# Performance work log

Measured on AMD Instinct MI355X. Metric: run time of the kernel, lower is better.

Reference implementation:

```python
import jax, jax.numpy as jnp
import numpy as np

B, Nq, Nk, R = 4, 1024, 1024, 256
NH, DK, DV = 8, 64, 64


def setup_inputs() -> dict:
    key = jax.random.key(0)
    ks = jax.random.split(key, 16)
    mk = lambda k, shape, s=1.0: jax.random.normal(k, shape, dtype=jnp.float32) * s
    inp = {
        'Q_real': mk(ks[0], (B, Nq, R)), 'Q_imag': mk(ks[1], (B, Nq, R)),
        'K_real': mk(ks[2], (B, Nk, R)), 'K_imag': mk(ks[3], (B, Nk, R)),
        'V_real': mk(ks[4], (B, Nk, R)), 'V_imag': mk(ks[5], (B, Nk, R)),
        'WQ_r': mk(ks[6], (NH * DK, R), 0.02), 'WQ_i': mk(ks[7], (NH * DK, R), 0.02),
        'WK_r': mk(ks[8], (NH * DK, R), 0.02), 'WK_i': mk(ks[9], (NH * DK, R), 0.02),
        'WV_r': mk(ks[10], (NH * DV, R), 0.02), 'WV_i': mk(ks[11], (NH * DV, R), 0.02),
        'WO_r': mk(ks[12], (R, NH * DV), 0.02), 'WO_i': mk(ks[13], (R, NH * DV), 0.02),
        'mask': jax.random.randint(ks[14], (B, Nk), 0, 2).astype(bool),
    }
    return inp


def _complex_linear(x, w_r, w_i):
    # x: complex [..., in]; weights real [out, in]. Same math as 4 real matmuls.
    w = (w_r + 1j * w_i).astype(jnp.complex64)
    return x @ w.T


def reference(Q_real, Q_imag, K_real, K_imag, V_real, V_imag,
              WQ_r, WQ_i, WK_r, WK_i, WV_r, WV_i, WO_r, WO_i, mask):
    Q = (Q_real + 1j * Q_imag).astype(jnp.complex64)
    K = (K_real + 1j * K_imag).astype(jnp.complex64)
    V = (V_real + 1j * V_imag).astype(jnp.complex64)

    Qp = _complex_linear(Q, WQ_r, WQ_i).reshape(B, Nq, NH, DK).transpose(0, 2, 1, 3)
    Kp = _complex_linear(K, WK_r, WK_i).reshape(B, Nk, NH, DK).transpose(0, 2, 1, 3)
    Vp = _complex_linear(V, WV_r, WV_i).reshape(B, Nk, NH, DV).transpose(0, 2, 1, 3)

    # complex scores [B, NH, Nq, Nk]; conj on K matches torch .conj().transpose
    scores = jnp.einsum('bhqd,bhkd->bhqk', Qp, jnp.conj(Kp)) / jnp.sqrt(jnp.float32(DK))
    scores_abs = jnp.abs(scores)

    m = mask[:, None, None, :]                    # [B,1,1,Nk]
    valid = jnp.any(mask, axis=-1)[:, None, None, None]  # [B,1,1,1] valid query rows
    masked = jnp.where(m, scores_abs, -jnp.inf)
    # avoid all -inf rows feeding softmax (those rows are zeroed afterwards)
    safe = jnp.where(valid, masked, 0.0)
    w = jax.nn.softmax(safe, axis=-1)
    w = jnp.where(valid, w, 0.0)

    attn = jnp.einsum('bhqk,bhkd->bhqd', w.astype(Vp.dtype), Vp)
    attn = attn.transpose(0, 2, 1, 3).reshape(B, Nq, NH * DV)
    return _complex_linear(attn, WO_r, WO_i)
```

## Files before the change

### kernel.cpp

```cpp
#include <hip/hip_runtime.h>
#include <hip/hip_bf16.h>

#define NBATCH 4
#define NSEQ   1024
#define RD     256
#define NHEAD  8
#define HD     64
#define NHD    512

typedef __attribute__((ext_vector_type(8))) short  short8;
typedef __attribute__((ext_vector_type(4))) short  short4v;
typedef __attribute__((ext_vector_type(4))) float  float4v;

#define MFMA16(a,b,c) __builtin_amdgcn_mfma_f32_16x16x32_bf16(a,b,c,0,0,0)

typedef const void __attribute__((address_space(1)))* gas_t;
typedef void __attribute__((address_space(3)))* las_t;
#define GLOAD16(g, l) __builtin_amdgcn_global_load_lds((gas_t)(g), (las_t)(l), 16, 0, 0)

static __device__ __forceinline__ short f2b(float f) {
    __hip_bfloat16 h = __float2bfloat16(f);
    union { __hip_bfloat16 h; short s; } u; u.h = h;
    return u.s;
}
static __device__ __forceinline__ void st4(short* dst, float4v v) {
    short4v p;
    p[0] = f2b(v[0]); p[1] = f2b(v[1]);
    p[2] = f2b(v[2]); p[3] = f2b(v[3]);
    *(short4v*)dst = p;
}

struct ConvArgs { const float* src[15]; short* dst[15]; int n4[15]; };

__global__ __launch_bounds__(256) void convert_bf16(ConvArgs ca)
{
    const int a = blockIdx.y;
    if (a == 14) {
        if (blockIdx.x != 0) return;
        __shared__ int isByteLayout;
        const int t = threadIdx.x;
        if (t == 0) isByteLayout = 0;
        __syncthreads();
        const int* mi = (const int*)ca.src[14];
        #pragma unroll
        for (int j = 0; j < 4; j++) {
            int v = mi[t*4 + j];
            if (v & ~1) isByteLayout = 1;
        }
        __syncthreads();
        const unsigned char* mb = (const unsigned char*)ca.src[14];
        unsigned char mv[16];
        int lc = 0;
        if (isByteLayout) {
            #pragma unroll
            for (int j = 0; j < 16; j++) { mv[j] = mb[t*16 + j] ? 1 : 0; lc += mv[j]; }
        } else {
            #pragma unroll
            for (int j = 0; j < 16; j++) { mv[j] = mi[t*16 + j] ? 1 : 0; lc += mv[j]; }
        }
        const int lane = t & 63, b = t >> 6;
        int sum = lc;
        #pragma unroll
        for (int d = 1; d < 64; d <<= 1) {
            int o = __shfl_up(sum, d, 64);
            if (lane >= d) sum += o;
        }
        int p = sum - lc;
        unsigned short* idxOut = (unsigned short*)ca.dst[14];
        int* cntOut = (int*)(idxOut + 4096);
        unsigned short* ib = idxOut + b*1024;
        #pragma unroll
        for (int j = 0; j < 16; j++)
            if (mv[j]) ib[p++] = (unsigned short)(lane*16 + j);
        if (lane == 63) cntOut[b] = sum;
        return;
    }
    if (a >= 2 && a <= 5) {
        const int t = threadIdx.x;
        const int r0 = blockIdx.x * 16;
        const int b  = r0 >> 10;
        __shared__ int isByteLayout;
        __shared__ unsigned short ib[1024];
        __shared__ int scnt;
        if (t == 0) isByteLayout = 0;
        __syncthreads();
        const int* mi = (const int*)ca.src[14];
        #pragma unroll
        for (int j = 0; j < 4; j++) {
            int v = mi[t*4 + j];
            if (v & ~1) isByteLayout = 1;
        }
        __syncthreads();
        if (t < 64) {
            const unsigned char* mb8 = (const unsigned char*)ca.src[14];
            unsigned char mv[16]; int lc = 0;
            if (isByteLayout) {
                #pragma unroll
                for (int j = 0; j < 16; j++) { mv[j] = mb8[b*1024 + t*16 + j] ? 1 : 0; lc += mv[j]; }
            } else {
                #pragma unroll
                for (int j = 0; j < 16; j++) { mv[j] = mi[b*1024 + t*16 + j] ? 1 : 0; lc += mv[j]; }
            }
            int sum = lc;
            #pragma unroll
            for (int d = 1; d < 64; d <<= 1) {
                int o = __shfl_up(sum, d, 64);
                if (t >= d) sum += o;
            }
            int p = sum - lc;
            #pragma unroll
            for (int j = 0; j < 16; j++)
                if (mv[j]) ib[p++] = (unsigned short)(t*16 + j);
            if (t == 63) scnt = sum;
        }
        __syncthreads();
        const int cb = scnt, L = (cb + 63) & ~63;
        const float* __restrict__ s = ca.src[a];
        short* __restrict__ d = ca.dst[a];
        const int jj = t >> 4, c = t & 15;
        const int j  = r0 + jj;
        const int jl = j & 1023;
        if (jl < L) {
            short* dp = d + (size_t)j*RD + c*4;
            if (jl < cb) {
                const float* sp = s + ((size_t)(b*NSEQ) + ib[jl])*RD + c*4;
                #pragma unroll
                for (int u = 0; u < 4; u++) {
                    float4v v = *(const float4v*)(sp + u*64);
                    st4(dp + u*64, v);
                }
            } else {
                short4v z = {0,0,0,0};
                #pragma unroll
                for (int u = 0; u < 4; u++) *(short4v*)(dp + u*64) = z;
            }
        }
        return;
    }
    const float* __restrict__ s = ca.src[a];
    short* __restrict__ d = ca.dst[a];
    const int n4 = ca.n4[a];
    for (int i = blockIdx.x*256 + threadIdx.x; i < n4; i += gridDim.x*256) {
        float4v v = *(const float4v*)(s + (size_t)i*4);
        st4(d + (size_t)i*4, v);
    }
}

struct ProjArgs {
    const short* Xr[3]; const short* Xi[3];
    const short* Wr[3]; const short* Wi[3];
    short* Yr[3]; short* Yi[3];
    const int* cnt;
};

__global__ __launch_bounds__(256) void cgemm_proj(ProjArgs pa)
{
    __shared__ __align__(16) char smemP[49152];
    short (*sX)[2][128][32] = (short(*)[2][128][32])smemP;
    short (*sW)[2][64][32]  = (short(*)[2][64][32])(smemP + 32768);

    const int wgid = blockIdx.x;
    const int flat = (wgid & 7) * 96 + (wgid >> 3);
    const int z    = flat % 3;
    const int rem  = flat / 3;
    const int nx = rem & 7, my = rem >> 3;
    const int n0 = nx * 64, m0 = my * 128;

    if (z >= 1) {
        int b  = m0 >> 10;
        int nb = m0 & 1023;
        int L  = (pa.cnt[b] + 63) & ~63;
        if (nb >= L) return;
    }
    const short* __restrict__ X_r = pa.Xr[z];
    const short* __restrict__ X_i = pa.Xi[z];
    const short* __restrict__ W_r = pa.Wr[z];
    const short* __restrict__ W_i = pa.Wi[z];
    short* __restrict__ Y_r = pa.Yr[z];
    short* __restrict__ Y_i = pa.Yi[z];
    const int transposeOut = (z == 2);

    const int tid  = threadIdx.x;
    const int lane = tid & 63, wave = tid >> 6;
    const int quad = lane >> 4, l16 = lane & 15;
    const int lrow = lane >> 2;
    const int scg  = (lane & 3) ^ (lrow & 3);

    const short nk = (short)0x8000;
    const short8 neg = {nk,nk,nk,nk,nk,nk,nk,nk};

    float4v zf = {0.f,0.f,0.f,0.f};
    float4v Yr[2][4], Yi[2][4];
    #pragma unroll
    for (int ms = 0; ms < 2; ms++)
        #pragma unroll
        for (int t = 0; t < 4; t++) { Yr[ms][t] = zf; Yi[ms][t] = zf; }

    #define PROJ_STAGE(kc, bf)                                                \
        if (wave < 2) {                                                       \
            const short* gp = wave ? X_i : X_r;                               \
            short* lp = &sX[bf][wave][0][0];                                  \
            _Pragma("unroll")                                                 \
            for (int j = 0; j < 8; j++)                                       \
                GLOAD16(gp + (size_t)(m0 + j*16 + lrow)*RD + (kc) + scg*8,    \
                        lp + j*512);                                          \
        } else {                                                              \
            const short* gp = (wave == 3) ? W_i : W_r;                        \
            short* lp = &sW[bf][wave - 2][0][0];                              \
            _Pragma("unroll")                                                 \
            for (int j = 0; j < 4; j++)                                       \
                GLOAD16(gp + (size_t)(n0 + j*16 + lrow)*RD + (kc) + scg*8,    \
                        lp + j*512);                                          \
        }

    PROJ_STAGE(0, 0);

    const int xsh = l16 & 3;
    for (int c = 0; c < 8; c++) {
        __syncthreads();
        if (c + 1 < 8) { PROJ_STAGE((c + 1)*32, (c + 1) & 1); }
        const int bf = c & 1;
        const int u = (quad ^ xsh) * 8;

        short8 fxr[2], fxi[2], fxin[2];
        #pragma unroll
        for (int ms = 0; ms < 2; ms++) {
            int row = wave*32 + ms*16 + l16;
            fxr[ms]  = *(short8*)&sX[bf][0][row][u];
            fxi[ms]  = *(short8*)&sX[bf][1][row][u];
            fxin[ms] = fxi[ms] ^ neg;
        }
        #pragma unroll
        for (int t = 0; t < 4; t++) {
            short8 wr = *(short8*)&sW[bf][0][t*16 + l16][u];
            short8 wi = *(short8*)&sW[bf][1][t*16 + l16][u];
            #pragma unroll
            for (int ms = 0; ms < 2; ms++) {
                Yr[ms][t] = MFMA16(fxr[ms],  wr, Yr[ms][t]);
                Yr[ms][t] = MFMA16(fxin[ms], wi, Yr[ms][t]);
                Yi[ms][t] = MFMA16(fxr[ms],  wi, Yi[ms][t]);
                Yi[ms][t] = MFMA16(fxi[ms],  wr, Yi[ms][t]);
            }
        }
    }
    #undef PROJ_STAGE

    const int b = m0 >> 10, h = n0 >> 6, nb = m0 & 1023;
    short* sT = (short*)smemP;
    const int PLSZ = transposeOut ? 8448 : 8704;
    __syncthreads();
    #pragma unroll
    for (int ms = 0; ms < 2; ms++)
        #pragma unroll
        for (int t = 0; t < 4; t++)
            #pragma unroll
            for (int r = 0; r < 4; r++) {
                int rr = wave*32 + ms*16 + quad*4 + r;
                int cc = t*16 + l16;
                if (!transposeOut) {
                    sT[rr*68 + cc]          = f2b(Yr[ms][t][r]);
                    sT[PLSZ + rr*68 + cc]   = f2b(Yi[ms][t][r]);
                } else {
                    sT[cc*132 + rr]         = f2b(Yr[ms][t][r]);
                    sT[PLSZ + cc*132 + rr]  = f2b(Yi[ms][t][r]);
                }
            }
    __syncthreads();
    short* Yp[2] = { Y_r, Y_i };
    #pragma unroll
    for (int p = 0; p < 2; p++) {
        #pragma unroll
        for (int it = 0; it < 4; it++) {
            int idx = it*256 + tid;
            int rr, c8;
            size_t o;
            const short* sp;
            if (!transposeOut) {
                rr = idx >> 3; c8 = (idx & 7)*8;
                sp = &sT[p*PLSZ + rr*68 + c8];
                o = (((size_t)(b*NHEAD + h))*NSEQ + nb + rr)*HD + c8;
            } else {
                rr = idx >> 4; c8 = (idx & 15)*8;
                sp = &sT[p*PLSZ + rr*132 + c8];
                o = (((size_t)(b*NHEAD + h))*HD + rr)*NSEQ + nb + c8;
            }
            short4v a = *(short4v*)sp;
            short4v bq = *(short4v*)(sp + 4);
            short8 v8 = { a[0],a[1],a[2],a[3], bq[0],bq[1],bq[2],bq[3] };
            *(short8*)&Yp[p][o] = v8;
        }
    }
}

__global__ __launch_bounds__(512) void attn_mfma(
    const short* __restrict__ Qp_r, const short* __restrict__ Qp_i,
    const short* __restrict__ Kp_r, const short* __restrict__ Kp_i,
    const short* __restrict__ Vp_r, const short* __restrict__ Vp_i,
    const int* __restrict__ cnt,
    short* __restrict__ Ar, short* __restrict__ Ai)
{
    __shared__ __align__(16) char smem[75776];
    short (*sP)[16][40] = (short(*)[16][40])(smem + 65536);

    const int tid  = threadIdx.x;
    const int lane = tid & 63, wave = tid >> 6;
    const int quad = lane >> 4, l16 = lane & 15;
    const int sw8  = l16 & 7;
    const int qstrip = wave >> 1;
    const int khalf  = wave & 1;
    const int qt = blockIdx.x >> 5;
    const int bh = blockIdx.x & 31;
    const int b  = bh >> 3, h = bh & 7;
    const size_t base = (size_t)bh * (NSEQ*HD);

    const int rsub = lane >> 3;
    const int colg = (lane & 7) ^ rsub;

    const int cb = cnt[b];
    const int nt = (cb + 63) >> 6;

    const int splane = wave >> 1;
    const short* sgp = (splane == 0) ? Kp_r : (splane == 1) ? Kp_i
                     : (splane == 2) ? Vp_r : Vp_i;
    const int sisV = (splane >= 2);
    const int soff = splane * 8192;

    const short nk = (short)0x8000;
    const short8 neg = {nk,nk,nk,nk,nk,nk,nk,nk};
    short8 fqr[2], fqi[2], fqrn[2];
    #pragma unroll
    for (int ds = 0; ds < 2; ds++) {
        size_t qo = base + (size_t)(qt*64 + qstrip*16 + l16)*HD + ds*32 + quad*8;
        fqr[ds]  = *(const short8*)&Qp_r[qo];
        fqi[ds]  = *(const short8*)&Qp_i[qo];
        fqrn[ds] = fqr[ds] ^ neg;
    }

    float4v zf = {0.f,0.f,0.f,0.f};
    float4v Or[4], Oi[4];
    float lrow[4];
    #pragma unroll
    for (int t = 0; t < 4; t++) { Or[t] = zf; Oi[t] = zf; }
    #pragma unroll
    for (int r = 0; r < 4; r++) lrow[r] = 0.f;

    const float C2 = 0.18033688f;

    if (nt > 0) {
        short* lp = (short*)(smem + soff);
        #pragma unroll
        for (int jj = 0; jj < 4; jj++) {
            int j = (wave & 1)*4 + jj;
            int row = j*8 + rsub;
            const short* g = sisV
                ? sgp + base + (size_t)row*NSEQ + colg*8
                : sgp + base + (size_t)row*HD + colg*8;
            GLOAD16(g, lp + j*512);
        }
    }

    for (int kt = 0; kt < nt; kt++) {
        __syncthreads();

        if (kt + 1 < nt) {
            const int kn = (kt + 1) * 64;
            short* lp = (short*)(smem + ((kt + 1) & 1)*32768 + soff);
            #pragma unroll
            for (int jj = 0; jj < 4; jj++) {
                int j = (wave & 1)*4 + jj;
                int row = j*8 + rsub;
                const short* g = sisV
                    ? sgp + base + (size_t)row*NSEQ + kn + colg*8
                    : sgp + base + (size_t)(kn + row)*HD + colg*8;
                GLOAD16(g, lp + j*512);
            }
        }

        const char* buf = smem + (kt & 1)*32768;
        short (*sK0)[64] = (short(*)[64])(buf);
        short (*sK1)[64] = (short(*)[64])(buf + 8192);
        short (*sV0)[64] = (short(*)[64])(buf + 16384);
        short (*sV1)[64] = (short(*)[64])(buf + 24576);
        const int k0 = kt*64;

        float4v Sr[2], Si[2];
        Sr[0] = zf; Sr[1] = zf; Si[0] = zf; Si[1] = zf;
        __builtin_amdgcn_s_setprio(1);
        #pragma unroll
        for (int t = 0; t < 2; t++)
            #pragma unroll
            for (int ds = 0; ds < 2; ds++) {
                int u = ((ds*4 + quad) ^ sw8) * 8;
                int krow = khalf*32 + t*16 + l16;
                short8 kr = *(short8*)&sK0[krow][u];
                short8 ki = *(short8*)&sK1[krow][u];
                Sr[t] = MFMA16(fqr[ds],  kr, Sr[t]);
                Sr[t] = MFMA16(fqi[ds],  ki, Sr[t]);
                Si[t] = MFMA16(fqi[ds],  kr, Si[t]);
                Si[t] = MFMA16(fqrn[ds], ki, Si[t]);
            }
        __builtin_amdgcn_s_setprio(0);

        #pragma unroll
        for (int t = 0; t < 2; t++) {
            bool mv = (k0 + khalf*32 + t*16 + l16) < cb;
            #pragma unroll
            for (int r = 0; r < 4; r++) {
                float a = Sr[t][r], c = Si[t][r];
                float x = fmaf(a, a, c*c);
                float s = __builtin_amdgcn_sqrtf(x);
                float e = mv ? __builtin_amdgcn_exp2f(C2 * s) : 0.f;
                lrow[r] += e;
                sP[wave][quad*4 + r][t*16 + l16] = f2b(e);
            }
        }

        {
            short8 fp = *(short8*)&sP[wave][l16][quad*8];
            __builtin_amdgcn_s_setprio(1);
            #pragma unroll
            for (int t = 0; t < 4; t++) {
                int u = ((khalf*4 + quad) ^ sw8) * 8;
                short8 vr = *(short8*)&sV0[t*16 + l16][u];
                short8 vi = *(short8*)&sV1[t*16 + l16][u];
                Or[t] = MFMA16(fp, vr, Or[t]);
                Oi[t] = MFMA16(fp, vi, Oi[t]);
            }
            __builtin_amdgcn_s_setprio(0);
        }
    }

    __syncthreads();
    float* sC = (float*)smem;
    float* sL = (float*)(smem + 32768);
    if (khalf == 1) {
        #pragma unroll
        for (int t = 0; t < 4; t++)
            #pragma unroll
            for (int r = 0; r < 4; r++) {
                int o8 = ((qstrip*4 + t)*64 + lane)*8 + r*2;
                sC[o8]     = Or[t][r];
                sC[o8 + 1] = Oi[t][r];
            }
        int lo = (qstrip*64 + lane)*4;
        #pragma unroll
        for (int r = 0; r < 4; r++) sL[lo + r] = lrow[r];
    }
    __syncthreads();
    if (khalf == 0) {
        #pragma unroll
        for (int t = 0; t < 4; t++)
            #pragma unroll
            for (int r = 0; r < 4; r++) {
                int o8 = ((qstrip*4 + t)*64 + lane)*8 + r*2;
                Or[t][r] += sC[o8];
                Oi[t][r] += sC[o8 + 1];
            }
        int lo = (qstrip*64 + lane)*4;
        float inv[4];
        #pragma unroll
        for (int r = 0; r < 4; r++) {
            float ls = lrow[r] + sL[lo + r];
            ls += __shfl_xor(ls, 1, 64);
            ls += __shfl_xor(ls, 2, 64);
            ls += __shfl_xor(ls, 4, 64);
            ls += __shfl_xor(ls, 8, 64);
            inv[r] = (ls > 0.f) ? 1.f/ls : 0.f;
        }
        #pragma unroll
        for (int t = 0; t < 4; t++)
            #pragma unroll
            for (int r = 0; r < 4; r++) {
                int q = qt*64 + qstrip*16 + quad*4 + r;
                int d = t*16 + l16;
                size_t o = ((size_t)(b*NSEQ + q))*NHD + h*HD + d;
                Ar[o] = f2b(Or[t][r] * inv[r]);
                Ai[o] = f2b(Oi[t][r] * inv[r]);
            }
    }
}

__global__ __launch_bounds__(256) void cgemm_out(
    const short* __restrict__ A_r, const short* __restrict__ A_i,
    const short* __restrict__ W_r, const short* __restrict__ W_i,
    float* __restrict__ Out, int writeImagPlane)
{
    __shared__ short sA[2][2][64][64];
    __shared__ short sW[2][2][32][64];
    const int tid  = threadIdx.x;
    const int lane = tid & 63, wave = tid >> 6;
    const int quad = lane >> 4, l16 = lane & 15;
    const int sw8  = l16 & 7;
    const int rsub = lane >> 3;
    const int colg = (lane & 7) ^ rsub;

    const int wgid = blockIdx.x;
    const int flat = (wgid & 7) * 64 + (wgid >> 3);
    const int n0 = (flat & 7) * 32, m0 = (flat >> 3) * 64;

    const short nk = (short)0x8000;
    const short8 neg = {nk,nk,nk,nk,nk,nk,nk,nk};

    float4v zf = {0.f,0.f,0.f,0.f};
    float4v Yr[2], Yi[2];
    #pragma unroll
    for (int t = 0; t < 2; t++) { Yr[t] = zf; Yi[t] = zf; }

    #define OUT_STAGE(kc, bf)                                                 \
        if (wave < 2) {                                                       \
            const short* gp = wave ? A_i : A_r;                               \
            short* lp = &sA[bf][wave][0][0];                                  \
            _Pragma("unroll")                                                 \
            for (int j = 0; j < 8; j++)                                       \
                GLOAD16(gp + (size_t)(m0 + j*8 + rsub)*NHD + (kc) + colg*8,   \
                        lp + j*512);                                          \
        } else {                                                              \
            const short* gp = (wave == 3) ? W_i : W_r;                        \
            short* lp = &sW[bf][wave - 2][0][0];                              \
            _Pragma("unroll")                                                 \
            for (int j = 0; j < 4; j++)                                       \
                GLOAD16(gp + (size_t)(n0 + j*8 + rsub)*NHD + (kc) + colg*8,   \
                        lp + j*512);                                          \
        }

    OUT_STAGE(0, 0);

    for (int c = 0; c < 8; c++) {
        __syncthreads();
        if (c + 1 < 8) { OUT_STAGE((c + 1)*64, (c + 1) & 1); }
        const int bf = c & 1;

        short8 far[2], fai[2], fain[2];
        #pragma unroll
        for (int ds = 0; ds < 2; ds++) {
            int u = ((ds*4 + quad) ^ sw8) * 8;
            far[ds]  = *(short8*)&sA[bf][0][wave*16 + l16][u];
            fai[ds]  = *(short8*)&sA[bf][1][wave*16 + l16][u];
            fain[ds] = fai[ds] ^ neg;
        }
        #pragma unroll
        for (int t = 0; t < 2; t++)
            #pragma unroll
            for (int ds = 0; ds < 2; ds++) {
                int u = ((ds*4 + quad) ^ sw8) * 8;
                short8 wr = *(short8*)&sW[bf][0][t*16 + l16][u];
                short8 wi = *(short8*)&sW[bf][1][t*16 + l16][u];
                Yr[t] = MFMA16(far[ds],  wr, Yr[t]);
                Yr[t] = MFMA16(fain[ds], wi, Yr[t]);
                Yi[t] = MFMA16(far[ds],  wi, Yi[t]);
                Yi[t] = MFMA16(fai[ds],  wr, Yi[t]);
            }
    }
    #undef OUT_STAGE

    const size_t TOT = (size_t)NBATCH * NSEQ * RD;
    #pragma unroll
    for (int t = 0; t < 2; t++)
        #pragma unroll
        for (int r = 0; r < 4; r++) {
            int row = m0 + wave*16 + quad*4 + r;
            int col = n0 + t*16 + l16;
            size_t o = (size_t)row*RD + col;
            Out[o] = Yr[t][r];
            if (writeImagPlane) Out[o + TOT] = Yi[t][r];
        }
}

extern "C" void kernel_launch(void* const* d_in, const int* in_sizes, int n_in,
                              void* d_out, int out_size, void* d_ws, size_t ws_size,
                              hipStream_t stream)
{
    float* out = (float*)d_out;

    const size_t P = (size_t)NBATCH * NHEAD * NSEQ * HD;
    const size_t H = (size_t)NBATCH * NSEQ * RD;
    const size_t WSZ = (size_t)NHD * RD;

    short* bws = (short*)d_ws;
    short* Qpr = bws + 0*P;  short* Qpi = bws + 1*P;
    short* Kpr = bws + 2*P;  short* Kpi = bws + 3*P;
    short* Vpr = bws + 4*P;  short* Vpi = bws + 5*P;
    short* conv = bws + 6*P;
    short* cX[6]; for (int i = 0; i < 6; i++) cX[i] = conv + i*H;
    short* cW[6]; for (int i = 0; i < 6; i++) cW[i] = conv + 6*H + i*WSZ;
    short* cWOr = conv + 6*H + 6*WSZ;
    short* cWOi = conv + 6*H + 7*WSZ;
    unsigned short* midx = (unsigned short*)(conv + 6*H + 8*WSZ);
    int* mcnt = (int*)(midx + 4096);
    short* Apr = conv;
    short* Api = conv + P;

    const size_t TOT = (size_t)NBATCH * NSEQ * RD;
    const int writeImagPlane = ((size_t)out_size >= 2*TOT) ? 1 : 0;

    ConvArgs ca;
    for (int i = 0; i < 6; i++) {
        ca.src[i] = (const float*)d_in[i];  ca.dst[i] = cX[i];  ca.n4[i] = (int)(H/4);
    }
    for (int i = 0; i < 6; i++) {
        ca.src[6+i] = (const float*)d_in[6+i]; ca.dst[6+i] = cW[i]; ca.n4[6+i] = (int)(WSZ/4);
    }
    ca.src[12] = (const float*)d_in[12]; ca.dst[12] = cWOr; ca.n4[12] = (int)(WSZ/4);
    ca.src[13] = (const float*)d_in[13]; ca.dst[13] = cWOi; ca.n4[13] = (int)(WSZ/4);
    ca.src[14] = (const float*)d_in[14]; ca.dst[14] = (short*)midx; ca.n4[14] = 0;

    ProjArgs pa;
    pa.Xr[0] = cX[0]; pa.Xi[0] = cX[1];
    pa.Xr[1] = cX[2]; pa.Xi[1] = cX[3];
    pa.Xr[2] = cX[4]; pa.Xi[2] = cX[5];
    pa.Wr[0] = cW[0]; pa.Wi[0] = cW[1];
    pa.Wr[1] = cW[2]; pa.Wi[1] = cW[3];
    pa.Wr[2] = cW[4]; pa.Wi[2] = cW[5];
    pa.Yr[0] = Qpr; pa.Yi[0] = Qpi;
    pa.Yr[1] = Kpr; pa.Yi[1] = Kpi;
    pa.Yr[2] = Vpr; pa.Yi[2] = Vpi;
    pa.cnt = mcnt;

    convert_bf16<<<dim3(256, 15), 256, 0, stream>>>(ca);
    cgemm_proj<<<dim3(768), 256, 0, stream>>>(pa);
    attn_mfma<<<dim3(512), 512, 0, stream>>>(Qpr, Qpi, Kpr, Kpi, Vpr, Vpi,
                                             mcnt, Apr, Api);
    cgemm_out<<<dim3(512), 256, 0, stream>>>(Apr, Api, cWOr, cWOi, out,
                                             writeImagPlane);
}
```

Before: 147.3 us.

## Load K/V fragments directly from global memory instead of LDS double-buffering

Drops the double-buffered LDS staging of K and V tiles, along with the per-tile block barrier. Each wave now reads its MFMA operands straight from global memory into registers. Shared memory shrinks to the per-wave P scratch and the reduction buffers, and a min-blocks hint of 4 is added to `launch_bounds` to raise occupancy. The cost is that loads are now issued without prefetch, so their latency is exposed, and the 4 query-strip wave pairs fetch the same K/V data redundantly through the caches. The occupancy hint may also cap registers tightly enough to cause spills.

```diff
diff --git a/kernel.cpp b/kernel.cpp
--- a/kernel.cpp
+++ b/kernel.cpp
@@ -292,20 +292,20 @@
     }
 }
 
-__global__ __launch_bounds__(512) void attn_mfma(
+__global__ __launch_bounds__(512, 4) void attn_mfma(
     const short* __restrict__ Qp_r, const short* __restrict__ Qp_i,
     const short* __restrict__ Kp_r, const short* __restrict__ Kp_i,
     const short* __restrict__ Vp_r, const short* __restrict__ Vp_i,
     const int* __restrict__ cnt,
     short* __restrict__ Ar, short* __restrict__ Ai)
 {
-    __shared__ __align__(16) char smem[75776];
-    short (*sP)[16][40] = (short(*)[16][40])(smem + 65536);
+    __shared__ float sC[8192];
+    __shared__ float sL[1024];
+    __shared__ short sP[8][16][40];
 
     const int tid  = threadIdx.x;
     const int lane = tid & 63, wave = tid >> 6;
     const int quad = lane >> 4, l16 = lane & 15;
-    const int sw8  = l16 & 7;
     const int qstrip = wave >> 1;
     const int khalf  = wave & 1;
     const int qt = blockIdx.x >> 5;
@@ -313,17 +313,8 @@
     const int b  = bh >> 3, h = bh & 7;
     const size_t base = (size_t)bh * (NSEQ*HD);
 
-    const int rsub = lane >> 3;
-    const int colg = (lane & 7) ^ rsub;
-
     const int cb = cnt[b];
     const int nt = (cb + 63) >> 6;
-
-    const int splane = wave >> 1;
-    const short* sgp = (splane == 0) ? Kp_r : (splane == 1) ? Kp_i
-                     : (splane == 2) ? Vp_r : Vp_i;
-    const int sisV = (splane >= 2);
-    const int soff = splane * 8192;
 
     const short nk = (short)0x8000;
     const short8 neg = {nk,nk,nk,nk,nk,nk,nk,nk};
@@ -346,59 +337,26 @@
 
     const float C2 = 0.18033688f;
 
-    if (nt > 0) {
-        short* lp = (short*)(smem + soff);
-        #pragma unroll
-        for (int jj = 0; jj < 4; jj++) {
-            int j = (wave & 1)*4 + jj;
-            int row = j*8 + rsub;
-            const short* g = sisV
-                ? sgp + base + (size_t)row*NSEQ + colg*8
-                : sgp + base + (size_t)row*HD + colg*8;
-            GLOAD16(g, lp + j*512);
-        }
-    }
-
     for (int kt = 0; kt < nt; kt++) {
-        __syncthreads();
-
-        if (kt + 1 < nt) {
-            const int kn = (kt + 1) * 64;
-            short* lp = (short*)(smem + ((kt + 1) & 1)*32768 + soff);
-            #pragma unroll
-            for (int jj = 0; jj < 4; jj++) {
-                int j = (wave & 1)*4 + jj;
-                int row = j*8 + rsub;
-                const short* g = sisV
-                    ? sgp + base + (size_t)row*NSEQ + kn + colg*8
-                    : sgp + base + (size_t)(kn + row)*HD + colg*8;
-                GLOAD16(g, lp + j*512);
-            }
-        }
-
-        const char* buf = smem + (kt & 1)*32768;
-        short (*sK0)[64] = (short(*)[64])(buf);
-        short (*sK1)[64] = (short(*)[64])(buf + 8192);
-        short (*sV0)[64] = (short(*)[64])(buf + 16384);
-        short (*sV1)[64] = (short(*)[64])(buf + 24576);
         const int k0 = kt*64;
 
         float4v Sr[2], Si[2];
         Sr[0] = zf; Sr[1] = zf; Si[0] = zf; Si[1] = zf;
         __builtin_amdgcn_s_setprio(1);
         #pragma unroll
-        for (int t = 0; t < 2; t++)
+        for (int t = 0; t < 2; t++) {
+            const size_t krO = base + (size_t)(k0 + khalf*32 + t*16 + l16)*HD;
             #pragma unroll
             for (int ds = 0; ds < 2; ds++) {
-                int u = ((ds*4 + quad) ^ sw8) * 8;
-                int krow = khalf*32 + t*16 + l16;
-                short8 kr = *(short8*)&sK0[krow][u];
-                short8 ki = *(short8*)&sK1[krow][u];
+                const int u = (ds*4 + quad)*8;
+                short8 kr = *(const short8*)&Kp_r[krO + u];
+                short8 ki = *(const short8*)&Kp_i[krO + u];
                 Sr[t] = MFMA16(fqr[ds],  kr, Sr[t]);
                 Sr[t] = MFMA16(fqi[ds],  ki, Sr[t]);
                 Si[t] = MFMA16(fqi[ds],  kr, Si[t]);
                 Si[t] = MFMA16(fqrn[ds], ki, Si[t]);
             }
+        }
         __builtin_amdgcn_s_setprio(0);
 
         #pragma unroll
@@ -417,12 +375,13 @@
 
         {
             short8 fp = *(short8*)&sP[wave][l16][quad*8];
+            const int kk = k0 + (khalf*4 + quad)*8;
             __builtin_amdgcn_s_setprio(1);
             #pragma unroll
             for (int t = 0; t < 4; t++) {
-                int u = ((khalf*4 + quad) ^ sw8) * 8;
-                short8 vr = *(short8*)&sV0[t*16 + l16][u];
-                short8 vi = *(short8*)&sV1[t*16 + l16][u];
+                const size_t vO = base + (size_t)(t*16 + l16)*NSEQ + kk;
+                short8 vr = *(const short8*)&Vp_r[vO];
+                short8 vi = *(const short8*)&Vp_i[vO];
                 Or[t] = MFMA16(fp, vr, Or[t]);
                 Oi[t] = MFMA16(fp, vi, Oi[t]);
             }
@@ -430,9 +389,6 @@
         }
     }
 
-    __syncthreads();
-    float* sC = (float*)smem;
-    float* sL = (float*)(smem + 32768);
     if (khalf == 1) {
         #pragma unroll
         for (int t = 0; t < 4; t++)
```

After: 192.4 us. 30.6% more time.

## Fuse output complex projection into attention kernel with atomic accumulation

Applied to the files above, without the earlier changes.

The separate cgemm_out kernel is removed. Each attention block now writes its normalized per-head output tile to shared memory and multiplies it by that head's slice of the complex output weights. Partial results are summed across heads with float atomicAdd into the output, which is zeroed by a memset beforehand. This drops the bf16 intermediate round-trip and one kernel launch, at the cost of atomic traffic (8 heads per element), a memset, weight loads straight from global memory, and a summation order that is no longer deterministic.

```diff
diff --git a/kernel.cpp b/kernel.cpp
--- a/kernel.cpp
+++ b/kernel.cpp
@@ -297,7 +297,8 @@
     const short* __restrict__ Kp_r, const short* __restrict__ Kp_i,
     const short* __restrict__ Vp_r, const short* __restrict__ Vp_i,
     const int* __restrict__ cnt,
-    short* __restrict__ Ar, short* __restrict__ Ai)
+    const short* __restrict__ WOr, const short* __restrict__ WOi,
+    float* __restrict__ Out, int writeImagPlane)
 {
     __shared__ __align__(16) char smem[75776];
     short (*sP)[16][40] = (short(*)[16][40])(smem + 65536);
@@ -433,6 +434,8 @@
     __syncthreads();
     float* sC = (float*)smem;
     float* sL = (float*)(smem + 32768);
+    short* sA2r = (short*)(smem + 36864);
+    short* sA2i = (short*)(smem + 45056);
     if (khalf == 1) {
         #pragma unroll
         for (int t = 0; t < 4; t++)
@@ -471,99 +474,60 @@
         for (int t = 0; t < 4; t++)
             #pragma unroll
             for (int r = 0; r < 4; r++) {
-                int q = qt*64 + qstrip*16 + quad*4 + r;
+                int q = qstrip*16 + quad*4 + r;
                 int d = t*16 + l16;
-                size_t o = ((size_t)(b*NSEQ + q))*NHD + h*HD + d;
-                Ar[o] = f2b(Or[t][r] * inv[r]);
-                Ai[o] = f2b(Oi[t][r] * inv[r]);
-            }
-    }
-}
-
-__global__ __launch_bounds__(256) void cgemm_out(
-    const short* __restrict__ A_r, const short* __restrict__ A_i,
-    const short* __restrict__ W_r, const short* __restrict__ W_i,
-    float* __restrict__ Out, int writeImagPlane)
-{
-    __shared__ short sA[2][2][64][64];
-    __shared__ short sW[2][2][32][64];
-    const int tid  = threadIdx.x;
-    const int lane = tid & 63, wave = tid >> 6;
-    const int quad = lane >> 4, l16 = lane & 15;
-    const int sw8  = l16 & 7;
-    const int rsub = lane >> 3;
-    const int colg = (lane & 7) ^ rsub;
-
-    const int wgid = blockIdx.x;
-    const int flat = (wgid & 7) * 64 + (wgid >> 3);
-    const int n0 = (flat & 7) * 32, m0 = (flat >> 3) * 64;
-
-    const short nk = (short)0x8000;
-    const short8 neg = {nk,nk,nk,nk,nk,nk,nk,nk};
-
-    float4v zf = {0.f,0.f,0.f,0.f};
-    float4v Yr[2], Yi[2];
-    #pragma unroll
-    for (int t = 0; t < 2; t++) { Yr[t] = zf; Yi[t] = zf; }
-
-    #define OUT_STAGE(kc, bf)                                                 \
-        if (wave < 2) {                                                       \
-            const short* gp = wave ? A_i : A_r;                               \
-            short* lp = &sA[bf][wave][0][0];                                  \
-            _Pragma("unroll")                                                 \
-            for (int j = 0; j < 8; j++)                                       \
-                GLOAD16(gp + (size_t)(m0 + j*8 + rsub)*NHD + (kc) + colg*8,   \
-                        lp + j*512);                                          \
-        } else {                                                              \
-            const short* gp = (wave == 3) ? W_i : W_r;                        \
-            short* lp = &sW[bf][wave - 2][0][0];                              \
-            _Pragma("unroll")                                                 \
-            for (int j = 0; j < 4; j++)                                       \
-                GLOAD16(gp + (size_t)(n0 + j*8 + rsub)*NHD + (kc) + colg*8,   \
-                        lp + j*512);                                          \
-        }
-
-    OUT_STAGE(0, 0);
-
-    for (int c = 0; c < 8; c++) {
-        __syncthreads();
-        if (c + 1 < 8) { OUT_STAGE((c + 1)*64, (c + 1) & 1); }
-        const int bf = c & 1;
-
-        short8 far[2], fai[2], fain[2];
-        #pragma unroll
-        for (int ds = 0; ds < 2; ds++) {
-            int u = ((ds*4 + quad) ^ sw8) * 8;
-            far[ds]  = *(short8*)&sA[bf][0][wave*16 + l16][u];
-            fai[ds]  = *(short8*)&sA[bf][1][wave*16 + l16][u];
-            fain[ds] = fai[ds] ^ neg;
-        }
-        #pragma unroll
-        for (int t = 0; t < 2; t++)
-            #pragma unroll
-            for (int ds = 0; ds < 2; ds++) {
-                int u = ((ds*4 + quad) ^ sw8) * 8;
-                short8 wr = *(short8*)&sW[bf][0][t*16 + l16][u];
-                short8 wi = *(short8*)&sW[bf][1][t*16 + l16][u];
-                Yr[t] = MFMA16(far[ds],  wr, Yr[t]);
-                Yr[t] = MFMA16(fain[ds], wi, Yr[t]);
-                Yi[t] = MFMA16(far[ds],  wi, Yi[t]);
-                Yi[t] = MFMA16(fai[ds],  wr, Yi[t]);
-            }
-    }
-    #undef OUT_STAGE
-
-    const size_t TOT = (size_t)NBATCH * NSEQ * RD;
-    #pragma unroll
-    for (int t = 0; t < 2; t++)
-        #pragma unroll
-        for (int r = 0; r < 4; r++) {
-            int row = m0 + wave*16 + quad*4 + r;
-            int col = n0 + t*16 + l16;
-            size_t o = (size_t)row*RD + col;
-            Out[o] = Yr[t][r];
-            if (writeImagPlane) Out[o + TOT] = Yi[t][r];
-        }
+                int ao = q*64 + ((d >> 3) ^ (q & 7))*8 + (d & 7);
+                sA2r[ao] = f2b(Or[t][r] * inv[r]);
+                sA2i[ao] = f2b(Oi[t][r] * inv[r]);
+            }
+    }
+    __syncthreads();
+
+    {
+        const size_t TOT = (size_t)NBATCH * NSEQ * RD;
+        float4v aR[4][2], aI[4][2];
+        #pragma unroll
+        for (int m = 0; m < 4; m++)
+            #pragma unroll
+            for (int nf = 0; nf < 2; nf++) { aR[m][nf] = zf; aI[m][nf] = zf; }
+        #pragma unroll
+        for (int ks = 0; ks < 2; ks++) {
+            short8 wr[2], wi[2];
+            #pragma unroll
+            for (int nf = 0; nf < 2; nf++) {
+                int n = wave*32 + nf*16 + l16;
+                size_t wo = (size_t)n*NHD + h*HD + ks*32 + quad*8;
+                wr[nf] = *(const short8*)&WOr[wo];
+                wi[nf] = *(const short8*)&WOi[wo];
+            }
+            #pragma unroll
+            for (int m = 0; m < 4; m++) {
+                int u = ((ks*4 + quad) ^ sw8) * 8;
+                short8 ar  = *(short8*)&sA2r[(m*16 + l16)*64 + u];
+                short8 ai  = *(short8*)&sA2i[(m*16 + l16)*64 + u];
+                short8 ain = ai ^ neg;
+                #pragma unroll
+                for (int nf = 0; nf < 2; nf++) {
+                    aR[m][nf] = MFMA16(ar,  wr[nf], aR[m][nf]);
+                    aR[m][nf] = MFMA16(ain, wi[nf], aR[m][nf]);
+                    aI[m][nf] = MFMA16(ar,  wi[nf], aI[m][nf]);
+                    aI[m][nf] = MFMA16(ai,  wr[nf], aI[m][nf]);
+                }
+            }
+        }
+        #pragma unroll
+        for (int m = 0; m < 4; m++)
+            #pragma unroll
+            for (int nf = 0; nf < 2; nf++)
+                #pragma unroll
+                for (int r = 0; r < 4; r++) {
+                    int row = qt*64 + m*16 + quad*4 + r;
+                    int col = wave*32 + nf*16 + l16;
+                    size_t o = ((size_t)(b*NSEQ + row))*RD + col;
+                    atomicAdd(&Out[o], aR[m][nf][r]);
+                    if (writeImagPlane) atomicAdd(&Out[o + TOT], aI[m][nf][r]);
+                }
+    }
 }
 
 extern "C" void kernel_launch(void* const* d_in, const int* in_sizes, int n_in,
@@ -587,8 +551,6 @@
     short* cWOi = conv + 6*H + 7*WSZ;
     unsigned short* midx = (unsigned short*)(conv + 6*H + 8*WSZ);
     int* mcnt = (int*)(midx + 4096);
-    short* Apr = conv;
-    short* Api = conv + P;
 
     const size_t TOT = (size_t)NBATCH * NSEQ * RD;
     const int writeImagPlane = ((size_t)out_size >= 2*TOT) ? 1 : 0;
@@ -616,10 +578,12 @@
     pa.Yr[2] = Vpr; pa.Yi[2] = Vpi;
     pa.cnt = mcnt;
 
+    hipMemsetAsync(out, 0, (size_t)(1 + writeImagPlane) * TOT * sizeof(float),
+                   stream);
+
     convert_bf16<<<dim3(256, 15), 256, 0, stream>>>(ca);
     cgemm_proj<<<dim3(768), 256, 0, stream>>>(pa);
     attn_mfma<<<dim3(512), 512, 0, stream>>>(Qpr, Qpi, Kpr, Kpi, Vpr, Vpi,
-                                             mcnt, Apr, Api);
-    cgemm_out<<<dim3(512), 256, 0, stream>>>(Apr, Api, cWOr, cWOi, out,
+                                             mcnt, cWOr, cWOi, out,
                                              writeImagPlane);
 }
```

Measured after the change: 171.2 us. 1.16x slower.
